# Kernel tuning notes

Measured on AMD Instinct MI355X. Metric: run time of the kernel, lower is better.

Reference implementation:

```python
import jax, jax.numpy as jnp
import numpy as np

N_S, N_G, D, K = 30000, 3000, 128, 16
SIGMA = 2.5
BOX = 60.0  # Angstrom box for random coordinates


def setup_inputs() -> dict:
    key = jax.random.key(0)
    ks = jax.random.split(key, 10)
    s = 1.0 / np.sqrt(D)
    return {
        'xs': jax.random.normal(ks[0], (N_S, D), jnp.float32),
        'xg': jax.random.normal(ks[1], (N_G, D), jnp.float32),
        'pos_s': jax.random.uniform(ks[2], (N_S, 3), jnp.float32) * BOX,
        'pos_g': jax.random.uniform(ks[3], (N_G, 3), jnp.float32) * BOX,
        'W_s_pre': jax.random.normal(ks[4], (D, D), jnp.float32) * s,
        'W_g_pre': jax.random.normal(ks[5], (D, D), jnp.float32) * s,
        'W_gs': jax.random.normal(ks[6], (D, D), jnp.float32) * s,
        'W_sg': jax.random.normal(ks[7], (D, D), jnp.float32) * s,
        'W_s_post': jax.random.normal(ks[8], (2 * D, D), jnp.float32) * s,
        'W_g_post': jax.random.normal(ks[9], (2 * D, D), jnp.float32) * s,
        'k': K,
    }


def reference(xs, xg, pos_s, pos_g, W_s_pre, W_g_pre, W_gs, W_sg, W_s_post, W_g_post, k):
    n_s, d = xs.shape
    # ---- compute_bipartite_graphs: knn of each graph node over surface nodes ----
    # squared pairwise distances via gemm form: (N_G, N_S)
    d2 = ((pos_g ** 2).sum(-1)[:, None] + (pos_s ** 2).sum(-1)[None, :]
          - 2.0 * pos_g @ pos_s.T)
    neg_d2, idx = jax.lax.top_k(-d2, k)          # idx: (N_G, K) surface neighbors
    w = jnp.exp(neg_d2 / (2.0 * SIGMA ** 2))     # RBF edge weight exp(-d^2/(2*sigma^2))
    # ---- pre blocks ----
    hs = xs @ W_s_pre                             # (N_S, D)
    hg = xg @ W_g_pre                             # (N_G, D)
    # ---- bp_gs block: graph -> surface weighted edge-conv (scatter-add) ----
    msg_gs = (hg @ W_gs)[:, None, :] * w[:, :, None]          # (N_G, K, D)
    xs_out = jnp.zeros((n_s, d), hs.dtype).at[idx.reshape(-1)].add(
        msg_gs.reshape(-1, d))
    # ---- bp_sg block: surface -> graph weighted edge-conv (gather-sum) ----
    xg_out = ((hs @ W_sg)[idx] * w[:, :, None]).sum(axis=1)   # (N_G, D)
    # ---- post blocks: combine pre features with message output ----
    xs_new = jax.nn.relu(jnp.concatenate([hs, xs_out], axis=-1) @ W_s_post)
    xg_new = jax.nn.relu(jnp.concatenate([hg, xg_out], axis=-1) @ W_g_post)
    return xs_new, xg_new
```

## Files before the change

### kernel.cpp

```cpp
#include <hip/hip_runtime.h>
#include <stdint.h>

#define N_S 30000
#define N_G 3000
#define DD  128
#define KK  16
#define NE  (N_G * KK)
#define NC  16
#define CELLS (NC * NC * NC)
#define CH  3.75f
#define CAP 32

using v8s = __attribute__((ext_vector_type(8))) short;
using v4f = __attribute__((ext_vector_type(4))) float;

__device__ int g_flag;

__device__ __forceinline__ float bf2f(unsigned short u) {
    union { unsigned int i; float f; } v; v.i = ((unsigned int)u) << 16; return v.f;
}
__device__ __forceinline__ unsigned short f2bf(float f) {
    union { float f; unsigned int i; } v; v.f = f;
    unsigned int x = v.i;
    return (unsigned short)((x + 0x7fffu + ((x >> 16) & 1u)) >> 16);
}
__device__ __forceinline__ float ldIn(const void* p, int i, int bf) {
    return bf ? bf2f(((const unsigned short*)p)[i]) : ((const float*)p)[i];
}
__device__ __forceinline__ void stOut(void* p, int i, float v, int bf) {
    if (bf) ((unsigned short*)p)[i] = f2bf(v);
    else    ((float*)p)[i] = v;
}
__device__ __forceinline__ int cellOf(float x) {
    int c = (int)(x * (1.0f / CH));
    if (c < 0) c = 0; if (c > NC - 1) c = NC - 1;
    return c;
}

__global__ void detect_kernel(const void* pos_g, int* __restrict__ ccnt,
                              int* __restrict__ novf) {
    const unsigned int* w = (const unsigned int*)pos_g;
    __shared__ int sv[256];
    const int t = threadIdx.x;
    for (int i = t; i < CELLS; i += 256) ccnt[i] = 0;
    if (t == 0) *novf = 0;
    int votes = 0;
    for (int i = t; i < 4500; i += 256) {
        unsigned int b = (w[i] >> 8) & 0xFFu;
        if (b >= 0x3Eu && b <= 0x42u) votes++;
    }
    sv[t] = votes; __syncthreads();
    for (int o = 128; o > 0; o >>= 1) {
        if (t < o) sv[t] += sv[t + o];
        __syncthreads();
    }
    if (t == 0) g_flag = (sv[0] > 2250) ? 1 : 0;
}

__global__ void grid_fill_kernel(const void* pos_s, int* __restrict__ ccnt,
                                 float4* __restrict__ scell,
                                 float4* __restrict__ ovf, int* __restrict__ novf) {
    const int p = blockIdx.x * 256 + threadIdx.x;
    if (p < N_S) {
        const int bf = g_flag;
        const float x = ldIn(pos_s, 3 * p + 0, bf);
        const float y = ldIn(pos_s, 3 * p + 1, bf);
        const float z = ldIn(pos_s, 3 * p + 2, bf);
        const int cid = (cellOf(x) * NC + cellOf(y)) * NC + cellOf(z);
        const int slot = atomicAdd(&ccnt[cid], 1);
        const float4 pt = make_float4(x, y, z, __int_as_float(p));
        if (slot < CAP) scell[cid * CAP + slot] = pt;
        else            ovf[atomicAdd(novf, 1)] = pt;
    }
}

__global__ __launch_bounds__(64) void knn_grid_kernel(
    const void* pos_g, const int* __restrict__ ccnt,
    const float4* __restrict__ scell,
    const float4* __restrict__ ovf, const int* __restrict__ novf_p,
    int* __restrict__ idx_out, float* __restrict__ w_out)
{
    __shared__ unsigned short map16[64 * CAP];
    __shared__ int s_pref[64];
    __shared__ int s_base[64];

    const int g = blockIdx.x;
    const int t = threadIdx.x;
    const int bf = g_flag;

    const float gxf = ldIn(pos_g, 3 * g + 0, bf);
    const float gyf = ldIn(pos_g, 3 * g + 1, bf);
    const float gzf = ldIn(pos_g, 3 * g + 2, bf);
    const double gx = (double)gxf, gy = (double)gyf, gz = (double)gzf;
    const int cx = cellOf(gxf), cy = cellOf(gyf), cz = cellOf(gzf);

    double bk[KK]; int bi[KK];
#pragma unroll
    for (int j = 0; j < KK; ++j) { bk[j] = 1e300; bi[j] = 0x7fffffff; }

    const int novf = *novf_p;
    for (int i = t; i < novf; i += 64) {
        const float4 cd = ovf[i];
        const double ddx = gx - (double)cd.x, ddy = gy - (double)cd.y, ddz = gz - (double)cd.z;
        const double d2 = ddx * ddx + ddy * ddy + ddz * ddz;
        const int sidx = __float_as_int(cd.w);
        if (d2 > bk[KK - 1] || (d2 == bk[KK - 1] && sidx > bi[KK - 1])) continue;
        double ck = d2; int ci2 = sidx;
#pragma unroll
        for (int j = 0; j < KK; ++j) {
            const bool less = (ck < bk[j]) || (ck == bk[j] && ci2 < bi[j]);
            const double nk = less ? ck : bk[j]; const int ni = less ? ci2 : bi[j];
            const double ok = less ? bk[j] : ck; const int oi = less ? bi[j] : ci2;
            bk[j] = nk; bi[j] = ni; ck = ok; ci2 = oi;
        }
    }

    bool done = false;
    for (int R = 1; R <= NC && !done; ++R) {
        const int S = 2 * R + 1;
        const int Scells = S * S * S;
        for (int cb = 0; cb < Scells; cb += 64) {
            const int ci = cb + t;
            int cnt = 0, base = 0;
            if (ci < Scells) {
                const int dz = ci % S - R;
                const int dy = (ci / S) % S - R;
                const int dx = ci / (S * S) - R;
                int ax = dx < 0 ? -dx : dx, ay = dy < 0 ? -dy : dy, az = dz < 0 ? -dz : dz;
                int cheb = ax > ay ? ax : ay; if (az > cheb) cheb = az;
                const bool want = (R == 1) ? true : (cheb == R);
                const int X = cx + dx, Y = cy + dy, Z = cz + dz;
                if (want && X >= 0 && X < NC && Y >= 0 && Y < NC && Z >= 0 && Z < NC) {
                    const int cid = (X * NC + Y) * NC + Z;
                    int c = ccnt[cid]; if (c > CAP) c = CAP;
                    cnt = c; base = cid * CAP;
                }
            }
            int incl = cnt;
            for (int d = 1; d < 64; d <<= 1) {
                int v = __shfl_up(incl, d);
                if (t >= d) incl += v;
            }
            const int total = __shfl(incl, 63);
            const int pref = incl - cnt;
            s_pref[t] = pref; s_base[t] = base;
            __syncthreads();
            for (int i = 0; i < cnt; ++i) map16[pref + i] = (unsigned short)t;
            __syncthreads();
            for (int pos = t; pos < total; pos += 64) {
                const int slot = map16[pos];
                const float4 cd = scell[s_base[slot] + (pos - s_pref[slot])];
                const double ddx = gx - (double)cd.x;
                const double ddy = gy - (double)cd.y;
                const double ddz = gz - (double)cd.z;
                const double d2 = ddx * ddx + ddy * ddy + ddz * ddz;
                const int sidx = __float_as_int(cd.w);
                if (d2 > bk[KK - 1]) continue;
                if (d2 == bk[KK - 1] && sidx > bi[KK - 1]) continue;
                double ck = d2; int ci2 = sidx;
#pragma unroll
                for (int j = 0; j < KK; ++j) {
                    const bool less = (ck < bk[j]) || (ck == bk[j] && ci2 < bi[j]);
                    const double nk = less ? ck : bk[j]; const int ni = less ? ci2 : bi[j];
                    const double ok = less ? bk[j] : ck; const int oi = less ? bi[j] : ci2;
                    bk[j] = nk; bi[j] = ni; ck = ok; ci2 = oi;
                }
            }
            __syncthreads();
        }
        double m = 1e300;
        if (cx - R > 0)      { double d = gx - (double)(cx - R) * 3.75; if (d < m) m = d; }
        if (cx + R < NC - 1) { double d = (double)(cx + R + 1) * 3.75 - gx; if (d < m) m = d; }
        if (cy - R > 0)      { double d = gy - (double)(cy - R) * 3.75; if (d < m) m = d; }
        if (cy + R < NC - 1) { double d = (double)(cy + R + 1) * 3.75 - gy; if (d < m) m = d; }
        if (cz - R > 0)      { double d = gz - (double)(cz - R) * 3.75; if (d < m) m = d; }
        if (cz + R < NC - 1) { double d = (double)(cz + R + 1) * 3.75 - gz; if (d < m) m = d; }
        if (m < 0.0) m = 0.0;
        const double m2 = m * m * (1.0 - 1e-12);
        int cntlt = 0;
#pragma unroll
        for (int j = 0; j < KK; ++j) cntlt += (bk[j] < m2) ? 1 : 0;
        for (int d = 1; d < 64; d <<= 1) cntlt += __shfl_xor(cntlt, d);
        if (cntlt >= KK) done = true;
    }

    for (int p = 0; p < KK; ++p) {
        double key = bk[0]; int sid = bi[0];
        for (int d = 1; d < 64; d <<= 1) {
            const double ok = __shfl_xor(key, d);
            const int    os = __shfl_xor(sid, d);
            if (ok < key || (ok == key && os < sid)) { key = ok; sid = os; }
        }
        if (t == 0) {
            idx_out[g * KK + p] = sid;
            w_out[g * KK + p] = expf((float)(-key) * (1.0f / 12.5f));
        }
        const bool win = (bk[0] == key) && (bi[0] == sid);
        if (win) {
#pragma unroll
            for (int j = 0; j < KK - 1; ++j) { bk[j] = bk[j + 1]; bi[j] = bi[j + 1]; }
            bk[KK - 1] = 1e300; bi[KK - 1] = 0x7fffffff;
        }
    }
}

__global__ __launch_bounds__(128) void pack_kernel(
    const void* Wsp, const void* Wgp, const void* Wgs, const void* Wsg,
    const void* Wspost, const void* Wgpost,
    unsigned short* __restrict__ wpk_ps, unsigned short* __restrict__ wpk_pg,
    unsigned short* __restrict__ wpk_cs, unsigned short* __restrict__ wpk_cg)
{
    __shared__ float row[DD];
    const int b = blockIdx.x, j = threadIdx.x, bf = g_flag;
    float v; unsigned short* dst; int k;
    if (b < 128) {
        k = b; v = ldIn(Wsp, k * DD + j, bf); dst = wpk_ps;
    } else if (b < 256) {
        k = b - 128; v = ldIn(Wgp, k * DD + j, bf); dst = wpk_pg;
    } else {
        const int which_g = (b >= 512);
        const int r = which_g ? (b - 512) : (b - 256);
        const void* W1 = which_g ? Wsg : Wgs;
        const void* Wp = which_g ? Wgpost : Wspost;
        dst = which_g ? wpk_cg : wpk_cs;
        k = r;
        if (r < 128) {
            v = ldIn(Wp, r * DD + j, bf);
        } else {
            row[j] = ldIn(W1, (r - 128) * DD + j, bf);
            __syncthreads();
            float acc = 0.f;
            for (int m = 0; m < DD; ++m) acc += row[m] * ldIn(Wp, (DD + m) * DD + j, bf);
            v = acc;
        }
    }
    const int ks = k >> 5, q = (k >> 3) & 3, i = k & 7;
    dst[((ks * 4 + q) * 128 + j) * 8 + i] = f2bf(v);
}

__device__ __forceinline__ v8s loadA(const void* A, size_t off, int mode, int bf) {
    if (mode == 0 || (mode == 2 && bf)) {
        return *(const v8s*)((const unsigned short*)A + off);
    }
    const float* f = (const float*)A + off;
    v8s r;
#pragma unroll
    for (int i = 0; i < 8; ++i) r[i] = (short)f2bf(f[i]);
    return r;
}

__global__ __launch_bounds__(256) void mfma_pre_kernel(
    const void* xs, const void* xg,
    const unsigned short* __restrict__ wpk_ps, const unsigned short* __restrict__ wpk_pg,
    unsigned short* __restrict__ hsb, unsigned short* __restrict__ hgb,
    float* __restrict__ xs_agg, int nbs)
{
    const int b = blockIdx.x;
    const void* A; const unsigned short* wpk; unsigned short* out; int M, m0;
    const bool is_s = (b < nbs);
    if (is_s) { A = xs; wpk = wpk_ps; out = hsb; M = N_S; m0 = b * 64; }
    else      { A = xg; wpk = wpk_pg; out = hgb; M = N_G; m0 = (b - nbs) * 64; }

    const int wave = threadIdx.x >> 6, lane = threadIdx.x & 63;
    const int q = lane >> 4, lm = lane & 15;
    const int mb = m0 + wave * 16;
    const int mrow = mb + lm;
    const bool valid = (mrow < M);
    const int bf = g_flag;

    v4f acc[8];
#pragma unroll
    for (int t = 0; t < 8; ++t) acc[t] = {0.f, 0.f, 0.f, 0.f};
    for (int ks = 0; ks < 4; ++ks) {
        v8s a = {0,0,0,0,0,0,0,0};
        if (valid) a = loadA(A, (size_t)mrow * 128 + ks * 32 + q * 8, 2, bf);
        const unsigned short* wb = wpk + (size_t)(ks * 4 + q) * 128 * 8;
#pragma unroll
        for (int t = 0; t < 8; ++t) {
            const v8s bfr = *(const v8s*)(wb + (t * 16 + lm) * 8);
            acc[t] = __builtin_amdgcn_mfma_f32_16x16x32_bf16(a, bfr, acc[t], 0, 0, 0);
        }
    }
#pragma unroll
    for (int t = 0; t < 8; ++t)
#pragma unroll
        for (int r = 0; r < 4; ++r) {
            const int row = mb + q * 4 + r;
            if (row < M) out[(size_t)row * 128 + t * 16 + lm] = f2bf(acc[t][r]);
        }
    if (is_s) {
        for (int i = threadIdx.x; i < 64 * 128; i += 256) {
            const int r = m0 + (i >> 7);
            if (r < N_S) xs_agg[(size_t)r * 128 + (i & 127)] = 0.f;
        }
    }
}

__global__ __launch_bounds__(128) void scatgath_kernel(
    const unsigned short* __restrict__ hsb, const unsigned short* __restrict__ hgb,
    const int* __restrict__ idx, const float* __restrict__ w,
    float* __restrict__ xs_agg, unsigned short* __restrict__ aggg)
{
    const int b = blockIdx.x, j = threadIdx.x;
    if (b < N_G) {
        const float m = bf2f(hgb[b * DD + j]);
#pragma unroll
        for (int k = 0; k < KK; ++k)
            atomicAdd(&xs_agg[(size_t)idx[b * KK + k] * DD + j], m * w[b * KK + k]);
    } else {
        const int g = b - N_G;
        float acc = 0.f;
#pragma unroll
        for (int k = 0; k < KK; ++k)
            acc += w[g * KK + k] * bf2f(hsb[(size_t)idx[g * KK + k] * DD + j]);
        aggg[g * DD + j] = f2bf(acc);
    }
}

__global__ __launch_bounds__(256) void mfma_post_kernel(
    const unsigned short* __restrict__ hsb, const float* __restrict__ xs_agg,
    const unsigned short* __restrict__ hgb, const unsigned short* __restrict__ aggg,
    const unsigned short* __restrict__ wpk_cs, const unsigned short* __restrict__ wpk_cg,
    void* out, int nbs)
{
    const int b = blockIdx.x;
    const void* A1; const void* A2; int mode2; const unsigned short* wpk;
    int M, m0, ooff;
    if (b < nbs) { A1 = hsb; A2 = xs_agg; mode2 = 1; wpk = wpk_cs; M = N_S; m0 = b * 64; ooff = 0; }
    else { A1 = hgb; A2 = aggg; mode2 = 0; wpk = wpk_cg; M = N_G; m0 = (b - nbs) * 64; ooff = N_S * DD; }

    const int wave = threadIdx.x >> 6, lane = threadIdx.x & 63;
    const int q = lane >> 4, lm = lane & 15;
    const int mb = m0 + wave * 16;
    const int mrow = mb + lm;
    const bool valid = (mrow < M);
    const int bf = g_flag;

    v4f acc[8];
#pragma unroll
    for (int t = 0; t < 8; ++t) acc[t] = {0.f, 0.f, 0.f, 0.f};
    for (int ks = 0; ks < 8; ++ks) {
        const int kk = ks * 32 + q * 8;
        v8s a = {0,0,0,0,0,0,0,0};
        if (valid) {
            if (kk < 128) a = loadA(A1, (size_t)mrow * 128 + kk, 0, bf);
            else          a = loadA(A2, (size_t)mrow * 128 + (kk - 128), mode2, bf);
        }
        const unsigned short* wb = wpk + (size_t)(ks * 4 + q) * 128 * 8;
#pragma unroll
        for (int t = 0; t < 8; ++t) {
            const v8s bfr = *(const v8s*)(wb + (t * 16 + lm) * 8);
            acc[t] = __builtin_amdgcn_mfma_f32_16x16x32_bf16(a, bfr, acc[t], 0, 0, 0);
        }
    }
#pragma unroll
    for (int t = 0; t < 8; ++t)
#pragma unroll
        for (int r = 0; r < 4; ++r) {
            const int row = mb + q * 4 + r;
            if (row < M) {
                float v = acc[t][r];
                if (v < 0.f) v = 0.f;
                stOut(out, ooff + row * DD + t * 16 + lm, v, bf);
            }
        }
}

extern "C" void kernel_launch(void* const* d_in, const int* in_sizes, int n_in,
                              void* d_out, int out_size, void* d_ws, size_t ws_size,
                              hipStream_t stream)
{
    const void* xs       = d_in[0];
    const void* xg       = d_in[1];
    const void* pos_s    = d_in[2];
    const void* pos_g    = d_in[3];
    const void* W_s_pre  = d_in[4];
    const void* W_g_pre  = d_in[5];
    const void* W_gs     = d_in[6];
    const void* W_sg     = d_in[7];
    const void* W_s_post = d_in[8];
    const void* W_g_post = d_in[9];
    (void)in_sizes; (void)n_in; (void)out_size; (void)ws_size;

    char* ws = (char*)d_ws;
    size_t off_b = 0;
    auto alloc = [&](size_t bytes) -> void* {
        void* p = ws + off_b;
        off_b = (off_b + bytes + 255) & ~((size_t)255);
        return p;
    };
    unsigned short* hsb    = (unsigned short*)alloc((size_t)N_S * DD * 2);
    unsigned short* hgb    = (unsigned short*)alloc((size_t)N_G * DD * 2);
    unsigned short* aggg   = (unsigned short*)alloc((size_t)N_G * DD * 2);
    float*          xs_agg = (float*) alloc((size_t)N_S * DD * 4);
    unsigned short* wpk_ps = (unsigned short*)alloc((size_t)DD * DD * 2);
    unsigned short* wpk_pg = (unsigned short*)alloc((size_t)DD * DD * 2);
    unsigned short* wpk_cs = (unsigned short*)alloc((size_t)2 * DD * DD * 2);
    unsigned short* wpk_cg = (unsigned short*)alloc((size_t)2 * DD * DD * 2);
    int*            idx    = (int*)   alloc((size_t)NE * 4);
    float*          w      = (float*) alloc((size_t)NE * 4);
    int*            ccnt   = (int*)   alloc((size_t)CELLS * 4);
    int*            novf   = (int*)   alloc(256);
    float4*         scell  = (float4*)alloc((size_t)CELLS * CAP * 16);
    float4*         ovf    = (float4*)alloc((size_t)N_S * 16);

    const int nbs = (N_S + 63) / 64;
    const int nbg = (N_G + 63) / 64;

    detect_kernel<<<1, 256, 0, stream>>>(pos_g, ccnt, novf);
    grid_fill_kernel<<<(N_S + 255) / 256, 256, 0, stream>>>(pos_s, ccnt, scell, ovf, novf);
    knn_grid_kernel<<<N_G, 64, 0, stream>>>(pos_g, ccnt, scell, ovf, novf, idx, w);
    pack_kernel<<<768, 128, 0, stream>>>(W_s_pre, W_g_pre, W_gs, W_sg,
                                         W_s_post, W_g_post,
                                         wpk_ps, wpk_pg, wpk_cs, wpk_cg);
    mfma_pre_kernel<<<nbs + nbg, 256, 0, stream>>>(xs, xg, wpk_ps, wpk_pg,
                                                   hsb, hgb, xs_agg, nbs);
    scatgath_kernel<<<2 * N_G, 128, 0, stream>>>(hsb, hgb, idx, w, xs_agg, aggg);
    mfma_post_kernel<<<nbs + nbg, 256, 0, stream>>>(hsb, xs_agg, hgb, aggg,
                                                    wpk_cs, wpk_cg, d_out, nbs);
}
```

Before: 194.9 us.

## Fuse grid fill with weight packing and kNN with pre-GEMM; per-wave kNN

Removes the separate dtype-detect kernel: each block now votes on 16 words of pos_g instead of 4500, and counters are zeroed with a memset. Grid filling and weight packing share one launch, and the kNN search shares a launch with the pre-projection MFMA tiles so they can overlap. kNN now runs one wave per graph node, four nodes per block. Each lane scans its own cell's points directly, replacing the shared-memory prefix compaction and its barriers. Float A-operands are loaded as float4 pairs. This cuts launch count and synchronization, at the cost of possible lane load imbalance in kNN and a weaker dtype-detection heuristic.

```diff
diff --git a/kernel.cpp b/kernel.cpp
--- a/kernel.cpp
+++ b/kernel.cpp
@@ -11,10 +11,15 @@
 #define CH  3.75f
 #define CAP 32
 
+#define FILL_BLOCKS 118
+#define PACK_BLOCKS 384
+#define KNN_BLOCKS  750
+#define NBS 469
+#define NBG 47
+#define NTILE (NBS + NBG)
+
 using v8s = __attribute__((ext_vector_type(8))) short;
 using v4f = __attribute__((ext_vector_type(4))) float;
-
-__device__ int g_flag;
 
 __device__ __forceinline__ float bf2f(unsigned short u) {
     union { unsigned int i; float f; } v; v.i = ((unsigned int)u) << 16; return v.f;
@@ -37,56 +42,24 @@
     return c;
 }
 
-__global__ void detect_kernel(const void* pos_g, int* __restrict__ ccnt,
-                              int* __restrict__ novf) {
+__device__ __forceinline__ int detectFlag(const void* pos_g) {
     const unsigned int* w = (const unsigned int*)pos_g;
-    __shared__ int sv[256];
-    const int t = threadIdx.x;
-    for (int i = t; i < CELLS; i += 256) ccnt[i] = 0;
-    if (t == 0) *novf = 0;
     int votes = 0;
-    for (int i = t; i < 4500; i += 256) {
-        unsigned int b = (w[i] >> 8) & 0xFFu;
-        if (b >= 0x3Eu && b <= 0x42u) votes++;
-    }
-    sv[t] = votes; __syncthreads();
-    for (int o = 128; o > 0; o >>= 1) {
-        if (t < o) sv[t] += sv[t + o];
-        __syncthreads();
-    }
-    if (t == 0) g_flag = (sv[0] > 2250) ? 1 : 0;
-}
-
-__global__ void grid_fill_kernel(const void* pos_s, int* __restrict__ ccnt,
-                                 float4* __restrict__ scell,
-                                 float4* __restrict__ ovf, int* __restrict__ novf) {
-    const int p = blockIdx.x * 256 + threadIdx.x;
-    if (p < N_S) {
-        const int bf = g_flag;
-        const float x = ldIn(pos_s, 3 * p + 0, bf);
-        const float y = ldIn(pos_s, 3 * p + 1, bf);
-        const float z = ldIn(pos_s, 3 * p + 2, bf);
-        const int cid = (cellOf(x) * NC + cellOf(y)) * NC + cellOf(z);
-        const int slot = atomicAdd(&ccnt[cid], 1);
-        const float4 pt = make_float4(x, y, z, __int_as_float(p));
-        if (slot < CAP) scell[cid * CAP + slot] = pt;
-        else            ovf[atomicAdd(novf, 1)] = pt;
-    }
-}
-
-__global__ __launch_bounds__(64) void knn_grid_kernel(
-    const void* pos_g, const int* __restrict__ ccnt,
-    const float4* __restrict__ scell,
-    const float4* __restrict__ ovf, const int* __restrict__ novf_p,
-    int* __restrict__ idx_out, float* __restrict__ w_out)
-{
-    __shared__ unsigned short map16[64 * CAP];
-    __shared__ int s_pref[64];
-    __shared__ int s_base[64];
-
-    const int g = blockIdx.x;
-    const int t = threadIdx.x;
-    const int bf = g_flag;
+#pragma unroll
+    for (int i = 0; i < 16; ++i) {
+        const unsigned int b = (w[i] >> 8) & 0xFFu;
+        votes += (b >= 0x3Eu && b <= 0x42u) ? 1 : 0;
+    }
+    return votes >= 8;
+}
+
+__device__ void knn_wave(int g, int bf, const void* pos_g,
+                         const int* __restrict__ ccnt,
+                         const float4* __restrict__ scell,
+                         const float4* __restrict__ ovf, int novf,
+                         int* __restrict__ idx_out, float* __restrict__ w_out)
+{
+    const int t = threadIdx.x & 63;
 
     const float gxf = ldIn(pos_g, 3 * g + 0, bf);
     const float gyf = ldIn(pos_g, 3 * g + 1, bf);
@@ -98,7 +71,6 @@
 #pragma unroll
     for (int j = 0; j < KK; ++j) { bk[j] = 1e300; bi[j] = 0x7fffffff; }
 
-    const int novf = *novf_p;
     for (int i = t; i < novf; i += 64) {
         const float4 cd = ovf[i];
         const double ddx = gx - (double)cd.x, ddy = gy - (double)cd.y, ddz = gz - (double)cd.z;
@@ -136,20 +108,8 @@
                     cnt = c; base = cid * CAP;
                 }
             }
-            int incl = cnt;
-            for (int d = 1; d < 64; d <<= 1) {
-                int v = __shfl_up(incl, d);
-                if (t >= d) incl += v;
-            }
-            const int total = __shfl(incl, 63);
-            const int pref = incl - cnt;
-            s_pref[t] = pref; s_base[t] = base;
-            __syncthreads();
-            for (int i = 0; i < cnt; ++i) map16[pref + i] = (unsigned short)t;
-            __syncthreads();
-            for (int pos = t; pos < total; pos += 64) {
-                const int slot = map16[pos];
-                const float4 cd = scell[s_base[slot] + (pos - s_pref[slot])];
+            for (int i = 0; i < cnt; ++i) {
+                const float4 cd = scell[base + i];
                 const double ddx = gx - (double)cd.x;
                 const double ddy = gy - (double)cd.y;
                 const double ddz = gz - (double)cd.z;
@@ -166,7 +126,6 @@
                     bk[j] = nk; bi[j] = ni; ck = ok; ci2 = oi;
                 }
             }
-            __syncthreads();
         }
         double m = 1e300;
         if (cx - R > 0)      { double d = gx - (double)(cx - R) * 3.75; if (d < m) m = d; }
@@ -204,76 +163,48 @@
     }
 }
 
-__global__ __launch_bounds__(128) void pack_kernel(
-    const void* Wsp, const void* Wgp, const void* Wgs, const void* Wsg,
-    const void* Wspost, const void* Wgpost,
-    unsigned short* __restrict__ wpk_ps, unsigned short* __restrict__ wpk_pg,
-    unsigned short* __restrict__ wpk_cs, unsigned short* __restrict__ wpk_cg)
-{
-    __shared__ float row[DD];
-    const int b = blockIdx.x, j = threadIdx.x, bf = g_flag;
-    float v; unsigned short* dst; int k;
-    if (b < 128) {
-        k = b; v = ldIn(Wsp, k * DD + j, bf); dst = wpk_ps;
-    } else if (b < 256) {
-        k = b - 128; v = ldIn(Wgp, k * DD + j, bf); dst = wpk_pg;
-    } else {
-        const int which_g = (b >= 512);
-        const int r = which_g ? (b - 512) : (b - 256);
-        const void* W1 = which_g ? Wsg : Wgs;
-        const void* Wp = which_g ? Wgpost : Wspost;
-        dst = which_g ? wpk_cg : wpk_cs;
-        k = r;
-        if (r < 128) {
-            v = ldIn(Wp, r * DD + j, bf);
-        } else {
-            row[j] = ldIn(W1, (r - 128) * DD + j, bf);
-            __syncthreads();
-            float acc = 0.f;
-            for (int m = 0; m < DD; ++m) acc += row[m] * ldIn(Wp, (DD + m) * DD + j, bf);
-            v = acc;
-        }
-    }
-    const int ks = k >> 5, q = (k >> 3) & 3, i = k & 7;
-    dst[((ks * 4 + q) * 128 + j) * 8 + i] = f2bf(v);
-}
-
-__device__ __forceinline__ v8s loadA(const void* A, size_t off, int mode, int bf) {
-    if (mode == 0 || (mode == 2 && bf)) {
-        return *(const v8s*)((const unsigned short*)A + off);
-    }
-    const float* f = (const float*)A + off;
+__device__ __forceinline__ v8s loadA_bf16(const unsigned short* p) {
+    return *(const v8s*)p;
+}
+__device__ __forceinline__ v8s loadA_f32v(const float* f) {
+    const float4 a = *(const float4*)f;
+    const float4 b = *(const float4*)(f + 4);
     v8s r;
-#pragma unroll
-    for (int i = 0; i < 8; ++i) r[i] = (short)f2bf(f[i]);
+    r[0] = (short)f2bf(a.x); r[1] = (short)f2bf(a.y);
+    r[2] = (short)f2bf(a.z); r[3] = (short)f2bf(a.w);
+    r[4] = (short)f2bf(b.x); r[5] = (short)f2bf(b.y);
+    r[6] = (short)f2bf(b.z); r[7] = (short)f2bf(b.w);
     return r;
 }
-
-__global__ __launch_bounds__(256) void mfma_pre_kernel(
-    const void* xs, const void* xg,
-    const unsigned short* __restrict__ wpk_ps, const unsigned short* __restrict__ wpk_pg,
-    unsigned short* __restrict__ hsb, unsigned short* __restrict__ hgb,
-    float* __restrict__ xs_agg, int nbs)
-{
-    const int b = blockIdx.x;
-    const void* A; const unsigned short* wpk; unsigned short* out; int M, m0;
-    const bool is_s = (b < nbs);
-    if (is_s) { A = xs; wpk = wpk_ps; out = hsb; M = N_S; m0 = b * 64; }
-    else      { A = xg; wpk = wpk_pg; out = hgb; M = N_G; m0 = (b - nbs) * 64; }
+__device__ __forceinline__ v8s loadA_raw(const void* A, size_t off, int bf) {
+    if (bf) return loadA_bf16((const unsigned short*)A + off);
+    return loadA_f32v((const float*)A + off);
+}
+
+__device__ void pre_tile(int task, int bf, const void* xs, const void* xg,
+                         const unsigned short* __restrict__ wpk_ps,
+                         const unsigned short* __restrict__ wpk_pg,
+                         unsigned short* __restrict__ hsb,
+                         unsigned short* __restrict__ hgb,
+                         float* __restrict__ xs_agg)
+{
+    const void* A; const unsigned short* wpk; unsigned short* outp; int M, m0;
+    const bool is_s = (task < NBS);
+    if (is_s) { A = xs; wpk = wpk_ps; outp = hsb; M = N_S; m0 = task * 64; }
+    else      { A = xg; wpk = wpk_pg; outp = hgb; M = N_G; m0 = (task - NBS) * 64; }
 
     const int wave = threadIdx.x >> 6, lane = threadIdx.x & 63;
     const int q = lane >> 4, lm = lane & 15;
     const int mb = m0 + wave * 16;
     const int mrow = mb + lm;
     const bool valid = (mrow < M);
-    const int bf = g_flag;
 
     v4f acc[8];
 #pragma unroll
     for (int t = 0; t < 8; ++t) acc[t] = {0.f, 0.f, 0.f, 0.f};
     for (int ks = 0; ks < 4; ++ks) {
         v8s a = {0,0,0,0,0,0,0,0};
-        if (valid) a = loadA(A, (size_t)mrow * 128 + ks * 32 + q * 8, 2, bf);
+        if (valid) a = loadA_raw(A, (size_t)mrow * 128 + ks * 32 + q * 8, bf);
         const unsigned short* wb = wpk + (size_t)(ks * 4 + q) * 128 * 8;
 #pragma unroll
         for (int t = 0; t < 8; ++t) {
@@ -286,7 +217,7 @@
 #pragma unroll
         for (int r = 0; r < 4; ++r) {
             const int row = mb + q * 4 + r;
-            if (row < M) out[(size_t)row * 128 + t * 16 + lm] = f2bf(acc[t][r]);
+            if (row < M) outp[(size_t)row * 128 + t * 16 + lm] = f2bf(acc[t][r]);
         }
     if (is_s) {
         for (int i = threadIdx.x; i < 64 * 128; i += 256) {
@@ -296,45 +227,25 @@
     }
 }
 
-__global__ __launch_bounds__(128) void scatgath_kernel(
-    const unsigned short* __restrict__ hsb, const unsigned short* __restrict__ hgb,
-    const int* __restrict__ idx, const float* __restrict__ w,
-    float* __restrict__ xs_agg, unsigned short* __restrict__ aggg)
-{
-    const int b = blockIdx.x, j = threadIdx.x;
-    if (b < N_G) {
-        const float m = bf2f(hgb[b * DD + j]);
-#pragma unroll
-        for (int k = 0; k < KK; ++k)
-            atomicAdd(&xs_agg[(size_t)idx[b * KK + k] * DD + j], m * w[b * KK + k]);
-    } else {
-        const int g = b - N_G;
-        float acc = 0.f;
-#pragma unroll
-        for (int k = 0; k < KK; ++k)
-            acc += w[g * KK + k] * bf2f(hsb[(size_t)idx[g * KK + k] * DD + j]);
-        aggg[g * DD + j] = f2bf(acc);
-    }
-}
-
-__global__ __launch_bounds__(256) void mfma_post_kernel(
-    const unsigned short* __restrict__ hsb, const float* __restrict__ xs_agg,
-    const unsigned short* __restrict__ hgb, const unsigned short* __restrict__ aggg,
-    const unsigned short* __restrict__ wpk_cs, const unsigned short* __restrict__ wpk_cg,
-    void* out, int nbs)
-{
-    const int b = blockIdx.x;
-    const void* A1; const void* A2; int mode2; const unsigned short* wpk;
+__device__ void post_tile(int task, int bf,
+                          const unsigned short* __restrict__ hsb,
+                          const float* __restrict__ xs_agg,
+                          const unsigned short* __restrict__ hgb,
+                          const unsigned short* __restrict__ aggg,
+                          const unsigned short* __restrict__ wpk_cs,
+                          const unsigned short* __restrict__ wpk_cg,
+                          void* out)
+{
+    const unsigned short* A1; const void* A2; int a2f32; const unsigned short* wpk;
     int M, m0, ooff;
-    if (b < nbs) { A1 = hsb; A2 = xs_agg; mode2 = 1; wpk = wpk_cs; M = N_S; m0 = b * 64; ooff = 0; }
-    else { A1 = hgb; A2 = aggg; mode2 = 0; wpk = wpk_cg; M = N_G; m0 = (b - nbs) * 64; ooff = N_S * DD; }
+    if (task < NBS) { A1 = hsb; A2 = xs_agg; a2f32 = 1; wpk = wpk_cs; M = N_S; m0 = task * 64; ooff = 0; }
+    else { A1 = hgb; A2 = aggg; a2f32 = 0; wpk = wpk_cg; M = N_G; m0 = (task - NBS) * 64; ooff = N_S * DD; }
 
     const int wave = threadIdx.x >> 6, lane = threadIdx.x & 63;
     const int q = lane >> 4, lm = lane & 15;
     const int mb = m0 + wave * 16;
     const int mrow = mb + lm;
     const bool valid = (mrow < M);
-    const int bf = g_flag;
 
     v4f acc[8];
 #pragma unroll
@@ -343,8 +254,9 @@
         const int kk = ks * 32 + q * 8;
         v8s a = {0,0,0,0,0,0,0,0};
         if (valid) {
-            if (kk < 128) a = loadA(A1, (size_t)mrow * 128 + kk, 0, bf);
-            else          a = loadA(A2, (size_t)mrow * 128 + (kk - 128), mode2, bf);
+            if (kk < 128)      a = loadA_bf16(A1 + (size_t)mrow * 128 + kk);
+            else if (a2f32)    a = loadA_f32v((const float*)A2 + (size_t)mrow * 128 + (kk - 128));
+            else               a = loadA_bf16((const unsigned short*)A2 + (size_t)mrow * 128 + (kk - 128));
         }
         const unsigned short* wb = wpk + (size_t)(ks * 4 + q) * 128 * 8;
 #pragma unroll
@@ -364,6 +276,112 @@
                 stOut(out, ooff + row * DD + t * 16 + lm, v, bf);
             }
         }
+}
+
+__global__ __launch_bounds__(256) void fill_pack_kernel(
+    const void* pos_s, const void* pos_g,
+    const void* Wsp, const void* Wgp, const void* Wgs, const void* Wsg,
+    const void* Wspost, const void* Wgpost,
+    int* __restrict__ ccnt, float4* __restrict__ scell,
+    float4* __restrict__ ovf, int* __restrict__ novf,
+    unsigned short* __restrict__ wpk_ps, unsigned short* __restrict__ wpk_pg,
+    unsigned short* __restrict__ wpk_cs, unsigned short* __restrict__ wpk_cg)
+{
+    const int bf = detectFlag(pos_g);
+    const int bid = blockIdx.x, tid = threadIdx.x;
+    if (bid < FILL_BLOCKS) {
+        const int p = bid * 256 + tid;
+        if (p < N_S) {
+            const float x = ldIn(pos_s, 3 * p + 0, bf);
+            const float y = ldIn(pos_s, 3 * p + 1, bf);
+            const float z = ldIn(pos_s, 3 * p + 2, bf);
+            const int cid = (cellOf(x) * NC + cellOf(y)) * NC + cellOf(z);
+            const int slot = atomicAdd(&ccnt[cid], 1);
+            const float4 pt = make_float4(x, y, z, __int_as_float(p));
+            if (slot < CAP) scell[cid * CAP + slot] = pt;
+            else            ovf[atomicAdd(novf, 1)] = pt;
+        }
+        return;
+    }
+    __shared__ float rows[256];
+    const int rt = bid - FILL_BLOCKS;
+    const int half = tid >> 7, j = tid & 127;
+    const int task = rt * 2 + half;
+    float v; unsigned short* dst; int k;
+    if (task < 128) { k = task; v = ldIn(Wsp, k * DD + j, bf); dst = wpk_ps; }
+    else if (task < 256) { k = task - 128; v = ldIn(Wgp, k * DD + j, bf); dst = wpk_pg; }
+    else {
+        const int which_g = (task >= 512);
+        const int r = which_g ? (task - 512) : (task - 256);
+        const void* W1 = which_g ? Wsg : Wgs;
+        const void* Wp = which_g ? Wgpost : Wspost;
+        dst = which_g ? wpk_cg : wpk_cs;
+        k = r;
+        if (r < 128) v = ldIn(Wp, r * DD + j, bf);
+        else {
+            rows[half * 128 + j] = ldIn(W1, (r - 128) * DD + j, bf);
+            __syncthreads();
+            float acc = 0.f;
+            for (int m = 0; m < DD; ++m)
+                acc += rows[half * 128 + m] * ldIn(Wp, (DD + m) * DD + j, bf);
+            v = acc;
+        }
+    }
+    const int ks = k >> 5, q = (k >> 3) & 3, i = k & 7;
+    dst[((ks * 4 + q) * 128 + j) * 8 + i] = f2bf(v);
+}
+
+__global__ __launch_bounds__(256) void knn_pre_kernel(
+    const void* xs, const void* xg, const void* pos_g,
+    const int* __restrict__ ccnt, const float4* __restrict__ scell,
+    const float4* __restrict__ ovf, const int* __restrict__ novf,
+    int* __restrict__ idx, float* __restrict__ w,
+    const unsigned short* __restrict__ wpk_ps,
+    const unsigned short* __restrict__ wpk_pg,
+    unsigned short* __restrict__ hsb, unsigned short* __restrict__ hgb,
+    float* __restrict__ xs_agg)
+{
+    const int bf = detectFlag(pos_g);
+    const int bid = blockIdx.x;
+    if (bid < KNN_BLOCKS) {
+        const int node = bid * 4 + (threadIdx.x >> 6);
+        knn_wave(node, bf, pos_g, ccnt, scell, ovf, *novf, idx, w);
+    } else {
+        pre_tile(bid - KNN_BLOCKS, bf, xs, xg, wpk_ps, wpk_pg, hsb, hgb, xs_agg);
+    }
+}
+
+__global__ __launch_bounds__(128) void scatgath_kernel(
+    const void* pos_g,
+    const unsigned short* __restrict__ hsb, const unsigned short* __restrict__ hgb,
+    const int* __restrict__ idx, const float* __restrict__ w,
+    float* __restrict__ xs_agg, unsigned short* __restrict__ aggg)
+{
+    const int b = blockIdx.x, j = threadIdx.x;
+    if (b < N_G) {
+        const float m = bf2f(hgb[b * DD + j]);
+#pragma unroll
+        for (int k = 0; k < KK; ++k)
+            atomicAdd(&xs_agg[(size_t)idx[b * KK + k] * DD + j], m * w[b * KK + k]);
+    } else {
+        const int g = b - N_G;
+        float acc = 0.f;
+#pragma unroll
+        for (int k = 0; k < KK; ++k)
+            acc += w[g * KK + k] * bf2f(hsb[(size_t)idx[g * KK + k] * DD + j]);
+        aggg[g * DD + j] = f2bf(acc);
+    }
+}
+
+__global__ __launch_bounds__(256) void mfma_post_kernel(
+    const void* pos_g,
+    const unsigned short* __restrict__ hsb, const float* __restrict__ xs_agg,
+    const unsigned short* __restrict__ hgb, const unsigned short* __restrict__ aggg,
+    const unsigned short* __restrict__ wpk_cs, const unsigned short* __restrict__ wpk_cg,
+    void* out)
+{
+    const int bf = detectFlag(pos_g);
+    post_tile(blockIdx.x, bf, hsb, xs_agg, hgb, aggg, wpk_cs, wpk_cg, out);
 }
 
 extern "C" void kernel_launch(void* const* d_in, const int* in_sizes, int n_in,
@@ -399,23 +417,24 @@
     unsigned short* wpk_cg = (unsigned short*)alloc((size_t)2 * DD * DD * 2);
     int*            idx    = (int*)   alloc((size_t)NE * 4);
     float*          w      = (float*) alloc((size_t)NE * 4);
-    int*            ccnt   = (int*)   alloc((size_t)CELLS * 4);
-    int*            novf   = (int*)   alloc(256);
+    int*            ccnt   = (int*)   alloc((size_t)CELLS * 4 + 4);
+    int*            novf   = ccnt + CELLS;
     float4*         scell  = (float4*)alloc((size_t)CELLS * CAP * 16);
     float4*         ovf    = (float4*)alloc((size_t)N_S * 16);
 
-    const int nbs = (N_S + 63) / 64;
-    const int nbg = (N_G + 63) / 64;
-
-    detect_kernel<<<1, 256, 0, stream>>>(pos_g, ccnt, novf);
-    grid_fill_kernel<<<(N_S + 255) / 256, 256, 0, stream>>>(pos_s, ccnt, scell, ovf, novf);
-    knn_grid_kernel<<<N_G, 64, 0, stream>>>(pos_g, ccnt, scell, ovf, novf, idx, w);
-    pack_kernel<<<768, 128, 0, stream>>>(W_s_pre, W_g_pre, W_gs, W_sg,
-                                         W_s_post, W_g_post,
-                                         wpk_ps, wpk_pg, wpk_cs, wpk_cg);
-    mfma_pre_kernel<<<nbs + nbg, 256, 0, stream>>>(xs, xg, wpk_ps, wpk_pg,
-                                                   hsb, hgb, xs_agg, nbs);
-    scatgath_kernel<<<2 * N_G, 128, 0, stream>>>(hsb, hgb, idx, w, xs_agg, aggg);
-    mfma_post_kernel<<<nbs + nbg, 256, 0, stream>>>(hsb, xs_agg, hgb, aggg,
-                                                    wpk_cs, wpk_cg, d_out, nbs);
-}
+    hipMemsetAsync(ccnt, 0, (size_t)CELLS * 4 + 4, stream);
+
+    fill_pack_kernel<<<FILL_BLOCKS + PACK_BLOCKS, 256, 0, stream>>>(
+        pos_s, pos_g, W_s_pre, W_g_pre, W_gs, W_sg, W_s_post, W_g_post,
+        ccnt, scell, ovf, novf, wpk_ps, wpk_pg, wpk_cs, wpk_cg);
+
+    knn_pre_kernel<<<KNN_BLOCKS + NTILE, 256, 0, stream>>>(
+        xs, xg, pos_g, ccnt, scell, ovf, novf, idx, w,
+        wpk_ps, wpk_pg, hsb, hgb, xs_agg);
+
+    scatgath_kernel<<<2 * N_G, 128, 0, stream>>>(pos_g, hsb, hgb, idx, w,
+                                                 xs_agg, aggg);
+
+    mfma_post_kernel<<<NTILE, 256, 0, stream>>>(pos_g, hsb, xs_agg, hgb, aggg,
+                                                wpk_cs, wpk_cg, d_out);
+}
```

After: 211.0 us. 8.2% more time.
